# Kernel optimization log

Measured on AMD Instinct MI355X. Metric: run time of the kernel, lower is better.

## Reference

```python
import jax, jax.numpy as jnp
import numpy as np

N = 102400   # total nodes (64 graphs x 1600 nodes)
G = 64       # graphs in batch
NPG = N // G
E = 1638400  # total edges (avg degree 16)
EPG = E // G


def _segmean(x, ids, num):
    s = jax.ops.segment_sum(x, ids, num_segments=num)
    c = jax.ops.segment_sum(jnp.ones((x.shape[0], 1), x.dtype), ids, num_segments=num)
    return s / jnp.maximum(c, 1.0)


def setup_inputs() -> dict:
    key = jax.random.key(0)
    ks = jax.random.split(key, 32)
    node_features = jax.random.normal(ks[0], (N, 60), jnp.float32)
    edge_features = jax.random.normal(ks[1], (E, 1), jnp.float32)
    node_graph = jnp.arange(N, dtype=jnp.int32) // NPG
    edge_graph = jnp.arange(E, dtype=jnp.int32) // EPG
    senders = edge_graph * NPG + jax.random.randint(ks[2], (E,), 0, NPG)
    receivers = edge_graph * NPG + jax.random.randint(ks[3], (E,), 0, NPG)

    def W(k, o, i):
        return (jax.random.normal(k, (o, i), jnp.float32) / np.sqrt(i)).astype(jnp.float32)

    def b(k, o):
        return (jax.random.uniform(k, (o,), jnp.float32) * 0.02 - 0.01).astype(jnp.float32)

    p = dict(
        node_features=node_features, edge_features=edge_features,
        senders=senders, receivers=receivers,
        node_graph=node_graph, edge_graph=edge_graph,
        # encoder: EdgeLinear(8, edge=1, sender=60)
        enc_Wee=W(ks[4], 8, 1), enc_Wes=W(ks[5], 8, 60), enc_be=b(ks[6], 8),
        # encoder: NodeLinear(16, incoming=8, node=60)
        enc_Wnn=W(ks[7], 16, 60), enc_Wni=W(ks[8], 16, 8), enc_bn=b(ks[9], 16),
        # encoder: GlobalLinear(4, edge=8, node=16)
        enc_Wge=W(ks[10], 4, 8), enc_Wgn=W(ks[11], 4, 16), enc_bg=b(ks[12], 4),
        # hidden: EdgeLinear(8, edge=8, sender=16, global=4)
        hid_Wee=W(ks[13], 8, 8), hid_Wes=W(ks[14], 8, 16), hid_Weg=W(ks[15], 8, 4), hid_be=b(ks[16], 8),
        # hidden: NodeLinear(16, node=16, incoming=8, global=4)
        hid_Wnn=W(ks[17], 16, 16), hid_Wni=W(ks[18], 16, 8), hid_Wng=W(ks[19], 16, 4), hid_bn=b(ks[20], 16),
        # hidden: GlobalLinear(4, edge=8, node=16, global=4)
        hid_Wge=W(ks[21], 4, 8), hid_Wgn=W(ks[22], 4, 16), hid_Wgg=W(ks[23], 4, 4), hid_bg=b(ks[24], 4),
        # readouts
        ro_Wn=W(ks[25], 1, 16), ro_bn=b(ks[26], 1),
        ro_Wg=W(ks[27], 1, 4), ro_bg=b(ks[28], 1),
    )
    return p


def reference(node_features, edge_features, senders, receivers, node_graph, edge_graph,
              enc_Wee, enc_Wes, enc_be, enc_Wnn, enc_Wni, enc_bn, enc_Wge, enc_Wgn, enc_bg,
              hid_Wee, hid_Wes, hid_Weg, hid_be, hid_Wnn, hid_Wni, hid_Wng, hid_bn,
              hid_Wge, hid_Wgn, hid_Wgg, hid_bg, ro_Wn, ro_bn, ro_Wg, ro_bg):
    hops = 1
    # ---- encoder GN block ----
    e = jax.nn.relu(edge_features @ enc_Wee.T + node_features[senders] @ enc_Wes.T + enc_be)  # [E,8]
    n = jax.nn.relu(node_features @ enc_Wnn.T + _segmean(e, receivers, N) @ enc_Wni.T + enc_bn)  # [N,16]
    g = jax.nn.relu(_segmean(e, edge_graph, G) @ enc_Wge.T + _segmean(n, node_graph, G) @ enc_Wgn.T + enc_bg)  # [G,4]
    # ---- hidden GN blocks (shared weights across hops) ----
    for _ in range(hops):
        e = jax.nn.relu(e @ hid_Wee.T + n[senders] @ hid_Wes.T + g[edge_graph] @ hid_Weg.T + hid_be)
        n = jax.nn.relu(n @ hid_Wnn.T + _segmean(e, receivers, N) @ hid_Wni.T + g[node_graph] @ hid_Wng.T + hid_bn)
        g = jax.nn.relu(_segmean(e, edge_graph, G) @ hid_Wge.T + _segmean(n, node_graph, G) @ hid_Wgn.T + g @ hid_Wgg.T + hid_bg)
    # ---- readouts ----
    nodes_out = jax.nn.sigmoid(n @ ro_Wn.T + ro_bn)    # [N,1]
    globals_out = jax.nn.sigmoid(g @ ro_Wg.T + ro_bg)  # [G,1]
    return nodes_out, globals_out
```

## Files before the change

### kernel.cpp

```cpp
#include <hip/hip_runtime.h>
#include <hip/hip_bf16.h>
#include <hip/hip_fp16.h>

#define NN   102400
#define NG   64
#define NPG  1600
#define NE   1638400
#define EPG  25600
#define EPC  (EPG / 4)

typedef unsigned int u32;
typedef unsigned short u16;

#define OFF_EDAT   0
#define OFF_SPROJ  (NE)
#define OFF_PNN    (NE + 8 * NN)
#define OFF_SPROJA (NE + 16 * NN)
#define OFF_DEG    (NE + 20 * NN)
#define OFF_START  (NE + 21 * NN)
#define OFF_H4C    (NE + 22 * NN)
#define OFF_GS     (NE + 26 * NN)
#define GS_ESUM1 0
#define GS_NSUM1 512
#define GS_ESUM2 1536
#define GS_NSUM2 2048
#define GS_G1    3072
#define GS_GPE   3328
#define GS_GPN   3840

struct H8 { __half2 a, b, c, d; };

__device__ __forceinline__ void unpack8_f4(const float4 v, float* o) {
    const __half2* h = reinterpret_cast<const __half2*>(&v);
    float2 t0 = __half22float2(h[0]), t1 = __half22float2(h[1]);
    float2 t2 = __half22float2(h[2]), t3 = __half22float2(h[3]);
    o[0]=t0.x; o[1]=t0.y; o[2]=t1.x; o[3]=t1.y; o[4]=t2.x; o[5]=t2.y; o[6]=t3.x; o[7]=t3.y;
}
__device__ __forceinline__ void unpack8(const H8 v, float* o) {
    float2 t0 = __half22float2(v.a), t1 = __half22float2(v.b);
    float2 t2 = __half22float2(v.c), t3 = __half22float2(v.d);
    o[0]=t0.x; o[1]=t0.y; o[2]=t1.x; o[3]=t1.y; o[4]=t2.x; o[5]=t2.y; o[6]=t3.x; o[7]=t3.y;
}
__device__ __forceinline__ H8 pack8(const float* v) {
    H8 r;
    r.a = __floats2half2_rn(v[0], v[1]); r.b = __floats2half2_rn(v[2], v[3]);
    r.c = __floats2half2_rn(v[4], v[5]); r.d = __floats2half2_rn(v[6], v[7]);
    return r;
}
__device__ __forceinline__ u16 f2bf(float f) {
    u32 u = __float_as_uint(f);
    return (u16)((u + 0x7fffu + ((u >> 16) & 1u)) >> 16);
}
__device__ __forceinline__ float wsum(float v) {
#pragma unroll
    for (int o = 32; o >= 1; o >>= 1) v += __shfl_xor(v, o);
    return v;
}
__device__ __forceinline__ float sigmoidf_(float x) { return 1.f / (1.f + expf(-x)); }

__global__ __launch_bounds__(512) void k_hist4(const int* __restrict__ rcv, int* __restrict__ h4) {
    __shared__ int h[NPG];
    const int g = blockIdx.x >> 2, c = blockIdx.x & 3;
    for (int i = threadIdx.x; i < NPG; i += 512) h[i] = 0;
    __syncthreads();
    const int base = g * EPG + c * EPC;
    for (int t = threadIdx.x; t < EPC; t += 512) atomicAdd(&h[rcv[base + t] - g * NPG], 1);
    __syncthreads();
    int* out = h4 + (size_t)(g * 4 + c) * NPG;
    for (int i = threadIdx.x; i < NPG; i += 512) out[i] = h[i];
}

__global__ __launch_bounds__(320) void k_scan(
    int* __restrict__ h4c, int* __restrict__ deg, int* __restrict__ start)
{
    __shared__ int part[320];
    const int g = blockIdx.x, tid = threadIdx.x;
    const int vb = tid * 5;
    int hc[5][4], d[5], pre[5];
    int ts = 0;
#pragma unroll
    for (int i = 0; i < 5; ++i) {
        const int v = vb + i;
#pragma unroll
        for (int c = 0; c < 4; ++c) hc[i][c] = h4c[(size_t)(g * 4 + c) * NPG + v];
        d[i] = hc[i][0] + hc[i][1] + hc[i][2] + hc[i][3];
        pre[i] = ts;
        ts += d[i];
    }
    part[tid] = ts;
    __syncthreads();
    for (int o = 1; o < 320; o <<= 1) {
        const int v = (tid >= o) ? part[tid - o] : 0;
        __syncthreads();
        part[tid] += v;
        __syncthreads();
    }
    const int off = g * EPG + part[tid] - ts;
#pragma unroll
    for (int i = 0; i < 5; ++i) {
        const int v = vb + i;
        const int st = off + pre[i];
        deg[g * NPG + v] = d[i];
        start[g * NPG + v] = st;
        int run = st;
#pragma unroll
        for (int c = 0; c < 4; ++c) {
            h4c[(size_t)(g * 4 + c) * NPG + v] = run;
            run += hc[i][c];
        }
    }
}

__global__ __launch_bounds__(512) void k_scatter4(
    const float* __restrict__ ef, const int* __restrict__ snd, const int* __restrict__ rcv,
    const int* __restrict__ h4c, u32* __restrict__ edat)
{
    __shared__ int cur[NPG];
    const int g = blockIdx.x >> 2, c = blockIdx.x & 3;
    const int* cb = h4c + (size_t)(g * 4 + c) * NPG;
    for (int i = threadIdx.x; i < NPG; i += 512) cur[i] = cb[i];
    __syncthreads();
    const int base = g * EPG + c * EPC;
    for (int t = threadIdx.x; t < EPC; t += 512) {
        const int e = base + t;
        const int r = rcv[e] - g * NPG;
        const int p = atomicAdd(&cur[r], 1);
        const u32 s = (u32)(snd[e] - g * NPG);
        edat[p] = (s << 16) | (u32)f2bf(ef[e]);
    }
}

__global__ __launch_bounds__(256) void k_node_pre(
    const float* __restrict__ nf,
    const float* __restrict__ Wes, const float* __restrict__ Wnn,
    const float* __restrict__ ebe, const float* __restrict__ ebn,
    __half* __restrict__ sproj, __half* __restrict__ pnn,
    __half* __restrict__ sprojAc, float* __restrict__ gs)
{
    __shared__ float wE[480], wN[960];
    for (int i = threadIdx.x; i < 480; i += 256) wE[i] = Wes[i];
    for (int i = threadIdx.x; i < 960; i += 256) wN[i] = Wnn[i];
    if (blockIdx.x == 0) {
        for (int i = threadIdx.x; i < 3072; i += 256) gs[i] = 0.f;
    }
    __syncthreads();
    const int v = blockIdx.x * 256 + threadIdx.x;
    const float4* row = reinterpret_cast<const float4*>(nf + (size_t)v * 60);
    float x[60];
#pragma unroll
    for (int i = 0; i < 15; ++i) {
        const float4 a = row[i];
        x[4 * i] = a.x; x[4 * i + 1] = a.y; x[4 * i + 2] = a.z; x[4 * i + 3] = a.w;
    }
    float pes[8], pn[16];
#pragma unroll
    for (int j = 0; j < 8; ++j) pes[j] = ebe[j];
#pragma unroll
    for (int j = 0; j < 16; ++j) pn[j] = ebn[j];
#pragma unroll
    for (int k = 0; k < 60; ++k) {
        const float xv = x[k];
#pragma unroll
        for (int j = 0; j < 8; ++j)  pes[j] = fmaf(xv, wE[j * 60 + k], pes[j]);
#pragma unroll
        for (int j = 0; j < 16; ++j) pn[j]  = fmaf(xv, wN[j * 60 + k], pn[j]);
    }
    const H8 pa = pack8(pes);
    reinterpret_cast<H8*>(sproj)[(size_t)v * 2] = pa;
    reinterpret_cast<H8*>(sprojAc)[v] = pa;
    H8* pp = reinterpret_cast<H8*>(pnn) + (size_t)v * 2;
    pp[0] = pack8(pn); pp[1] = pack8(pn + 8);
}

__global__ __launch_bounds__(256) void k_enc4(
    const int* __restrict__ deg, const int* __restrict__ start, const u32* __restrict__ edat,
    const __half* __restrict__ sprojAc,
    __half* __restrict__ sproj, __half* __restrict__ pnn,
    const float* __restrict__ eWee, const float* __restrict__ eWni,
    const float* __restrict__ hWes, const float* __restrict__ hWnn,
    float* __restrict__ esum, float* __restrict__ nsum)
{
    __shared__ float wNI[128], wES[128], wNN2[256];
    const int tid = threadIdx.x, lane = tid & 63;
    for (int i = tid; i < 128; i += 256) { wNI[i] = eWni[i]; wES[i] = hWes[i]; }
    wNN2[tid] = hWnn[tid];
    __syncthreads();
    const int v = blockIdx.x * 256 + tid;
    const int g = v / NPG;
    float wee[8];
#pragma unroll
    for (int j = 0; j < 8; ++j) wee[j] = eWee[j];
    const int dg = deg[v];
    const int st = start[v];
    const int aend = st + dg;
    float m[8];
#pragma unroll
    for (int j = 0; j < 8; ++j) m[j] = 0.f;
    const float4* hbA = reinterpret_cast<const float4*>(sprojAc) + (size_t)g * NPG;

    for (int i = st & ~3; i < aend; i += 4) {
        const uint4 w4 = *reinterpret_cast<const uint4*>(edat + i);
        const u32 w[4] = {w4.x, w4.y, w4.z, w4.w};
        float4 A[4];
#pragma unroll
        for (int j = 0; j < 4; ++j) A[j] = hbA[w[j] >> 16];
#pragma unroll
        for (int j = 0; j < 4; ++j) {
            const int idx = i + j;
            const float val = (idx >= st && idx < aend) ? 1.f : 0.f;
            const float f = __uint_as_float((w[j] & 0xffffu) << 16);
            float pv[8]; unpack8_f4(A[j], pv);
#pragma unroll
            for (int k = 0; k < 8; ++k) m[k] += val * fmaxf(0.f, fmaf(f, wee[k], pv[k]));
        }
    }
#pragma unroll
    for (int j = 0; j < 8; ++j) {
        const float s = wsum(m[j]);
        if (lane == 0) atomicAdd(&esum[g * 8 + j], s);
    }
    const float ic = 1.f / fmaxf((float)dg, 1.f);
    float mk[8];
#pragma unroll
    for (int k = 0; k < 8; ++k) mk[k] = m[k] * ic;
    H8* pp = reinterpret_cast<H8*>(pnn) + (size_t)v * 2;
    float pn[16]; unpack8(pp[0], pn); unpack8(pp[1], pn + 8);
    float n1[16];
#pragma unroll
    for (int j = 0; j < 16; ++j) {
        float x = pn[j];
#pragma unroll
        for (int k = 0; k < 8; ++k) x = fmaf(mk[k], wNI[j * 8 + k], x);
        n1[j] = fmaxf(0.f, x);
    }
    float pe[8];
#pragma unroll
    for (int o = 0; o < 8; ++o) {
        float x = 0.f;
#pragma unroll
        for (int j = 0; j < 16; ++j) x = fmaf(n1[j], wES[o * 16 + j], x);
        pe[o] = x;
    }
    reinterpret_cast<H8*>(sproj)[(size_t)v * 2 + 1] = pack8(pe);
    float pw[16];
#pragma unroll
    for (int o = 0; o < 16; ++o) {
        float x = 0.f;
#pragma unroll
        for (int j = 0; j < 16; ++j) x = fmaf(n1[j], wNN2[o * 16 + j], x);
        pw[o] = x;
    }
    pp[0] = pack8(pw); pp[1] = pack8(pw + 8);
#pragma unroll
    for (int j = 0; j < 16; ++j) {
        const float s = wsum(n1[j]);
        if (lane == 0) atomicAdd(&nsum[g * 16 + j], s);
    }
}

__global__ void k_glob_enc(
    const float* __restrict__ esum1, const float* __restrict__ nsum1,
    const float* __restrict__ Wge, const float* __restrict__ Wgn, const float* __restrict__ bg,
    const float* __restrict__ hWeg, const float* __restrict__ hWng,
    float* __restrict__ g1, float* __restrict__ gpe, float* __restrict__ gpn)
{
    const int g = threadIdx.x;
    if (g >= NG) return;
    float gv[4];
#pragma unroll
    for (int o = 0; o < 4; ++o) {
        float x = bg[o];
#pragma unroll
        for (int k = 0; k < 8; ++k)  x = fmaf(esum1[g * 8 + k] * (1.f / EPG), Wge[o * 8 + k], x);
#pragma unroll
        for (int k = 0; k < 16; ++k) x = fmaf(nsum1[g * 16 + k] * (1.f / NPG), Wgn[o * 16 + k], x);
        gv[o] = fmaxf(0.f, x);
        g1[g * 4 + o] = gv[o];
    }
#pragma unroll
    for (int j = 0; j < 8; ++j) {
        float x = 0.f;
#pragma unroll
        for (int o = 0; o < 4; ++o) x = fmaf(gv[o], hWeg[j * 4 + o], x);
        gpe[g * 8 + j] = x;
    }
#pragma unroll
    for (int j = 0; j < 16; ++j) {
        float x = 0.f;
#pragma unroll
        for (int o = 0; o < 4; ++o) x = fmaf(gv[o], hWng[j * 4 + o], x);
        gpn[g * 16 + j] = x;
    }
}

__global__ __launch_bounds__(256) void k_hid4(
    const int* __restrict__ deg, const int* __restrict__ start, const u32* __restrict__ edat,
    const __half* __restrict__ sproj, const __half* __restrict__ pnn,
    const float* __restrict__ eWee,
    const float* __restrict__ hWee, const float* __restrict__ hbe, const float* __restrict__ gpe,
    const float* __restrict__ hWni, const float* __restrict__ hbn, const float* __restrict__ gpn,
    const float* __restrict__ roWn, const float* __restrict__ robn,
    float* __restrict__ esum, float* __restrict__ nsum, float* __restrict__ outn)
{
    __shared__ float w2[64], wNI[128], rW[16];
    const int tid = threadIdx.x, lane = tid & 63;
    for (int i = tid; i < 128; i += 256) wNI[i] = hWni[i];
    if (tid < 64) w2[tid] = hWee[tid];
    if (tid < 16) rW[tid] = roWn[tid];
    __syncthreads();
    const int v = blockIdx.x * 256 + tid;
    const int g = v / NPG;
    float wee[8], add2[8];
#pragma unroll
    for (int j = 0; j < 8; ++j) { wee[j] = eWee[j]; add2[j] = gpe[g * 8 + j] + hbe[j]; }
    const int dg = deg[v];
    const int st = start[v];
    const int aend = st + dg;
    float m2[8];
#pragma unroll
    for (int j = 0; j < 8; ++j) m2[j] = 0.f;
    const float4* hb4 = reinterpret_cast<const float4*>(sproj) + (size_t)g * NPG * 2;

    for (int i = st & ~3; i < aend; i += 4) {
        const uint4 w4 = *reinterpret_cast<const uint4*>(edat + i);
        const u32 w[4] = {w4.x, w4.y, w4.z, w4.w};
        float4 A[4], B[4];
#pragma unroll
        for (int j = 0; j < 4; ++j) {
            const size_t so = (size_t)(w[j] >> 16) * 2;
            A[j] = hb4[so]; B[j] = hb4[so + 1];
        }
#pragma unroll
        for (int j = 0; j < 4; ++j) {
            const int idx = i + j;
            const float val = (idx >= st && idx < aend) ? 1.f : 0.f;
            const float f = __uint_as_float((w[j] & 0xffffu) << 16);
            float pv[8], qv[8];
            unpack8_f4(A[j], pv); unpack8_f4(B[j], qv);
            float e1[8];
#pragma unroll
            for (int k = 0; k < 8; ++k) e1[k] = fmaxf(0.f, fmaf(f, wee[k], pv[k]));
#pragma unroll
            for (int k = 0; k < 8; ++k) {
                float x = qv[k] + add2[k];
#pragma unroll
                for (int kk = 0; kk < 8; ++kk) x = fmaf(e1[kk], w2[k * 8 + kk], x);
                m2[k] += val * fmaxf(0.f, x);
            }
        }
    }
#pragma unroll
    for (int j = 0; j < 8; ++j) {
        const float s = wsum(m2[j]);
        if (lane == 0) atomicAdd(&esum[g * 8 + j], s);
    }
    const float ic = 1.f / fmaxf((float)dg, 1.f);
    float mk[8];
#pragma unroll
    for (int k = 0; k < 8; ++k) mk[k] = m2[k] * ic;
    const H8* pp = reinterpret_cast<const H8*>(pnn) + (size_t)v * 2;
    float pn[16]; unpack8(pp[0], pn); unpack8(pp[1], pn + 8);
    float z = robn[0];
    float n2[16];
#pragma unroll
    for (int j = 0; j < 16; ++j) {
        float x = pn[j] + gpn[g * 16 + j] + hbn[j];
#pragma unroll
        for (int k = 0; k < 8; ++k) x = fmaf(mk[k], wNI[j * 8 + k], x);
        n2[j] = fmaxf(0.f, x);
        z = fmaf(n2[j], rW[j], z);
    }
    outn[v] = sigmoidf_(z);
#pragma unroll
    for (int j = 0; j < 16; ++j) {
        const float s = wsum(n2[j]);
        if (lane == 0) atomicAdd(&nsum[g * 16 + j], s);
    }
}

__global__ void k_glob_hid(
    const float* __restrict__ esum2, const float* __restrict__ nsum2, const float* __restrict__ g1,
    const float* __restrict__ hWge, const float* __restrict__ hWgn,
    const float* __restrict__ hWgg, const float* __restrict__ hbg,
    const float* __restrict__ roWg, const float* __restrict__ robg,
    float* __restrict__ outg)
{
    const int g = threadIdx.x;
    if (g >= NG) return;
    float gv[4];
#pragma unroll
    for (int o = 0; o < 4; ++o) {
        float x = hbg[o];
#pragma unroll
        for (int k = 0; k < 8; ++k)  x = fmaf(esum2[g * 8 + k] * (1.f / EPG), hWge[o * 8 + k], x);
#pragma unroll
        for (int k = 0; k < 16; ++k) x = fmaf(nsum2[g * 16 + k] * (1.f / NPG), hWgn[o * 16 + k], x);
#pragma unroll
        for (int k = 0; k < 4; ++k)  x = fmaf(g1[g * 4 + k], hWgg[o * 4 + k], x);
        gv[o] = fmaxf(0.f, x);
    }
    float z = robg[0];
#pragma unroll
    for (int o = 0; o < 4; ++o) z = fmaf(gv[o], roWg[o], z);
    outg[g] = sigmoidf_(z);
}

extern "C" void kernel_launch(void* const* d_in, const int* in_sizes, int n_in,
                              void* d_out, int out_size, void* d_ws, size_t ws_size,
                              hipStream_t stream)
{
    const float* nf   = (const float*)d_in[0];
    const float* ef   = (const float*)d_in[1];
    const int*   snd  = (const int*)d_in[2];
    const int*   rcv  = (const int*)d_in[3];
    const float* eWee = (const float*)d_in[6];
    const float* eWes = (const float*)d_in[7];
    const float* ebe  = (const float*)d_in[8];
    const float* eWnn = (const float*)d_in[9];
    const float* eWni = (const float*)d_in[10];
    const float* ebn  = (const float*)d_in[11];
    const float* eWge = (const float*)d_in[12];
    const float* eWgn = (const float*)d_in[13];
    const float* ebg  = (const float*)d_in[14];
    const float* hWee = (const float*)d_in[15];
    const float* hWes = (const float*)d_in[16];
    const float* hWeg = (const float*)d_in[17];
    const float* hbe  = (const float*)d_in[18];
    const float* hWnn = (const float*)d_in[19];
    const float* hWni = (const float*)d_in[20];
    const float* hWng = (const float*)d_in[21];
    const float* hbn  = (const float*)d_in[22];
    const float* hWge = (const float*)d_in[23];
    const float* hWgn = (const float*)d_in[24];
    const float* hWgg = (const float*)d_in[25];
    const float* hbg  = (const float*)d_in[26];
    const float* roWn = (const float*)d_in[27];
    const float* robn = (const float*)d_in[28];
    const float* roWg = (const float*)d_in[29];
    const float* robg = (const float*)d_in[30];

    float*  ws     = (float*)d_ws;
    u32*    edat   = (u32*)(ws + OFF_EDAT);
    __half* sproj  = (__half*)(ws + OFF_SPROJ);
    __half* pnn    = (__half*)(ws + OFF_PNN);
    __half* sprojA = (__half*)(ws + OFF_SPROJA);
    int*    deg    = (int*)(ws + OFF_DEG);
    int*    start  = (int*)(ws + OFF_START);
    int*    h4c    = (int*)(ws + OFF_H4C);
    float*  gs     = ws + OFF_GS;
    float* esum1 = gs + GS_ESUM1;
    float* nsum1 = gs + GS_NSUM1;
    float* esum2 = gs + GS_ESUM2;
    float* nsum2 = gs + GS_NSUM2;
    float* g1    = gs + GS_G1;
    float* gpe   = gs + GS_GPE;
    float* gpn   = gs + GS_GPN;
    float* out   = (float*)d_out;

    k_hist4<<<NG * 4, 512, 0, stream>>>(rcv, h4c);
    k_scan<<<NG, 320, 0, stream>>>(h4c, deg, start);
    k_scatter4<<<NG * 4, 512, 0, stream>>>(ef, snd, rcv, h4c, edat);
    k_node_pre<<<NN / 256, 256, 0, stream>>>(nf, eWes, eWnn, ebe, ebn, sproj, pnn, sprojA, gs);
    k_enc4<<<NN / 256, 256, 0, stream>>>(deg, start, edat, sprojA, sproj, pnn,
                                         eWee, eWni, hWes, hWnn, esum1, nsum1);
    k_glob_enc<<<1, 64, 0, stream>>>(esum1, nsum1, eWge, eWgn, ebg, hWeg, hWng, g1, gpe, gpn);
    k_hid4<<<NN / 256, 256, 0, stream>>>(deg, start, edat, sproj, pnn,
                                         eWee, hWee, hbe, gpe, hWni, hbn, gpn,
                                         roWn, robn, esum2, nsum2, out);
    k_glob_hid<<<1, 64, 0, stream>>>(esum2, nsum2, g1, hWge, hWgn, hWgg, hbg, roWg, robg, out + NN);
}
```

Before: 128.0 us.

## Stage per-graph sender projections in LDS for edge aggregation kernels

Blocks are remapped so each covers 200 nodes of a single graph (8 blocks per graph). Each block first copies that graph's sender projection table (1600 or 3200 float4) into shared memory, and the per-edge gathers then read LDS instead of global memory. The aim is to replace scattered global and L2 gathers with LDS reads. The cost is 56 idle threads per block, a large LDS footprint (about 51 KB in the hidden kernel) that limits occupancy, and the same table being loaded redundantly by 8 blocks per graph.

```diff
diff --git a/kernel.cpp b/kernel.cpp
--- a/kernel.cpp
+++ b/kernel.cpp
@@ -8,6 +8,7 @@
 #define NE   1638400
 #define EPG  25600
 #define EPC  (EPG / 4)
+#define NPC  200
 
 typedef unsigned int u32;
 typedef unsigned short u16;
@@ -172,7 +173,7 @@
     pp[0] = pack8(pn); pp[1] = pack8(pn + 8);
 }
 
-__global__ __launch_bounds__(256) void k_enc4(
+__global__ __launch_bounds__(256) void k_enc5(
     const int* __restrict__ deg, const int* __restrict__ start, const u32* __restrict__ edat,
     const __half* __restrict__ sprojAc,
     __half* __restrict__ sproj, __half* __restrict__ pnn,
@@ -180,30 +181,33 @@
     const float* __restrict__ hWes, const float* __restrict__ hWnn,
     float* __restrict__ esum, float* __restrict__ nsum)
 {
+    __shared__ float4 sA[NPG];
     __shared__ float wNI[128], wES[128], wNN2[256];
     const int tid = threadIdx.x, lane = tid & 63;
+    const int g = blockIdx.x >> 3, ch = blockIdx.x & 7;
+    const float4* hbA = reinterpret_cast<const float4*>(sprojAc) + (size_t)g * NPG;
+    for (int i = tid; i < NPG; i += 256) sA[i] = hbA[i];
     for (int i = tid; i < 128; i += 256) { wNI[i] = eWni[i]; wES[i] = hWes[i]; }
     wNN2[tid] = hWnn[tid];
     __syncthreads();
-    const int v = blockIdx.x * 256 + tid;
-    const int g = v / NPG;
     float wee[8];
 #pragma unroll
     for (int j = 0; j < 8; ++j) wee[j] = eWee[j];
-    const int dg = deg[v];
-    const int st = start[v];
+    const bool act = tid < NPC;
+    const int v = g * NPG + ch * NPC + (act ? tid : 0);
+    const int dg = act ? deg[v] : 0;
+    const int st = act ? start[v] : g * EPG;
     const int aend = st + dg;
     float m[8];
 #pragma unroll
     for (int j = 0; j < 8; ++j) m[j] = 0.f;
-    const float4* hbA = reinterpret_cast<const float4*>(sprojAc) + (size_t)g * NPG;
 
     for (int i = st & ~3; i < aend; i += 4) {
         const uint4 w4 = *reinterpret_cast<const uint4*>(edat + i);
         const u32 w[4] = {w4.x, w4.y, w4.z, w4.w};
         float4 A[4];
 #pragma unroll
-        for (int j = 0; j < 4; ++j) A[j] = hbA[w[j] >> 16];
+        for (int j = 0; j < 4; ++j) A[j] = sA[w[j] >> 16];
 #pragma unroll
         for (int j = 0; j < 4; ++j) {
             const int idx = i + j;
@@ -223,34 +227,43 @@
     float mk[8];
 #pragma unroll
     for (int k = 0; k < 8; ++k) mk[k] = m[k] * ic;
-    H8* pp = reinterpret_cast<H8*>(pnn) + (size_t)v * 2;
-    float pn[16]; unpack8(pp[0], pn); unpack8(pp[1], pn + 8);
+    float pn[16];
+    if (act) {
+        const H8* pp = reinterpret_cast<const H8*>(pnn) + (size_t)v * 2;
+        unpack8(pp[0], pn); unpack8(pp[1], pn + 8);
+    } else {
+#pragma unroll
+        for (int j = 0; j < 16; ++j) pn[j] = 0.f;
+    }
     float n1[16];
 #pragma unroll
     for (int j = 0; j < 16; ++j) {
         float x = pn[j];
 #pragma unroll
         for (int k = 0; k < 8; ++k) x = fmaf(mk[k], wNI[j * 8 + k], x);
-        n1[j] = fmaxf(0.f, x);
-    }
-    float pe[8];
-#pragma unroll
-    for (int o = 0; o < 8; ++o) {
-        float x = 0.f;
-#pragma unroll
-        for (int j = 0; j < 16; ++j) x = fmaf(n1[j], wES[o * 16 + j], x);
-        pe[o] = x;
-    }
-    reinterpret_cast<H8*>(sproj)[(size_t)v * 2 + 1] = pack8(pe);
-    float pw[16];
-#pragma unroll
-    for (int o = 0; o < 16; ++o) {
-        float x = 0.f;
-#pragma unroll
-        for (int j = 0; j < 16; ++j) x = fmaf(n1[j], wNN2[o * 16 + j], x);
-        pw[o] = x;
-    }
-    pp[0] = pack8(pw); pp[1] = pack8(pw + 8);
+        n1[j] = act ? fmaxf(0.f, x) : 0.f;
+    }
+    if (act) {
+        float pe[8];
+#pragma unroll
+        for (int o = 0; o < 8; ++o) {
+            float x = 0.f;
+#pragma unroll
+            for (int j = 0; j < 16; ++j) x = fmaf(n1[j], wES[o * 16 + j], x);
+            pe[o] = x;
+        }
+        reinterpret_cast<H8*>(sproj)[(size_t)v * 2 + 1] = pack8(pe);
+        float pw[16];
+#pragma unroll
+        for (int o = 0; o < 16; ++o) {
+            float x = 0.f;
+#pragma unroll
+            for (int j = 0; j < 16; ++j) x = fmaf(n1[j], wNN2[o * 16 + j], x);
+            pw[o] = x;
+        }
+        H8* pp = reinterpret_cast<H8*>(pnn) + (size_t)v * 2;
+        pp[0] = pack8(pw); pp[1] = pack8(pw + 8);
+    }
 #pragma unroll
     for (int j = 0; j < 16; ++j) {
         const float s = wsum(n1[j]);
@@ -293,7 +306,7 @@
     }
 }
 
-__global__ __launch_bounds__(256) void k_hid4(
+__global__ __launch_bounds__(256) void k_hid5(
     const int* __restrict__ deg, const int* __restrict__ start, const u32* __restrict__ edat,
     const __half* __restrict__ sproj, const __half* __restrict__ pnn,
     const float* __restrict__ eWee,
@@ -302,24 +315,27 @@
     const float* __restrict__ roWn, const float* __restrict__ robn,
     float* __restrict__ esum, float* __restrict__ nsum, float* __restrict__ outn)
 {
+    __shared__ float4 sAB[NPG * 2];
     __shared__ float w2[64], wNI[128], rW[16];
     const int tid = threadIdx.x, lane = tid & 63;
+    const int g = blockIdx.x >> 3, ch = blockIdx.x & 7;
+    const float4* f4sp = reinterpret_cast<const float4*>(sproj) + (size_t)g * NPG * 2;
+    for (int i = tid; i < NPG * 2; i += 256) sAB[i] = f4sp[i];
     for (int i = tid; i < 128; i += 256) wNI[i] = hWni[i];
     if (tid < 64) w2[tid] = hWee[tid];
-    if (tid < 16) rW[tid] = roWn[tid];
-    __syncthreads();
-    const int v = blockIdx.x * 256 + tid;
-    const int g = v / NPG;
+    if (tid >= 64 && tid < 80) rW[tid - 64] = roWn[tid - 64];
+    __syncthreads();
     float wee[8], add2[8];
 #pragma unroll
     for (int j = 0; j < 8; ++j) { wee[j] = eWee[j]; add2[j] = gpe[g * 8 + j] + hbe[j]; }
-    const int dg = deg[v];
-    const int st = start[v];
+    const bool act = tid < NPC;
+    const int v = g * NPG + ch * NPC + (act ? tid : 0);
+    const int dg = act ? deg[v] : 0;
+    const int st = act ? start[v] : g * EPG;
     const int aend = st + dg;
     float m2[8];
 #pragma unroll
     for (int j = 0; j < 8; ++j) m2[j] = 0.f;
-    const float4* hb4 = reinterpret_cast<const float4*>(sproj) + (size_t)g * NPG * 2;
 
     for (int i = st & ~3; i < aend; i += 4) {
         const uint4 w4 = *reinterpret_cast<const uint4*>(edat + i);
@@ -327,8 +343,8 @@
         float4 A[4], B[4];
 #pragma unroll
         for (int j = 0; j < 4; ++j) {
-            const size_t so = (size_t)(w[j] >> 16) * 2;
-            A[j] = hb4[so]; B[j] = hb4[so + 1];
+            const int so = (int)(w[j] >> 16) * 2;
+            A[j] = sAB[so]; B[j] = sAB[so + 1];
         }
 #pragma unroll
         for (int j = 0; j < 4; ++j) {
@@ -358,8 +374,14 @@
     float mk[8];
 #pragma unroll
     for (int k = 0; k < 8; ++k) mk[k] = m2[k] * ic;
-    const H8* pp = reinterpret_cast<const H8*>(pnn) + (size_t)v * 2;
-    float pn[16]; unpack8(pp[0], pn); unpack8(pp[1], pn + 8);
+    float pn[16];
+    if (act) {
+        const H8* pp = reinterpret_cast<const H8*>(pnn) + (size_t)v * 2;
+        unpack8(pp[0], pn); unpack8(pp[1], pn + 8);
+    } else {
+#pragma unroll
+        for (int j = 0; j < 16; ++j) pn[j] = 0.f;
+    }
     float z = robn[0];
     float n2[16];
 #pragma unroll
@@ -367,10 +389,10 @@
         float x = pn[j] + gpn[g * 16 + j] + hbn[j];
 #pragma unroll
         for (int k = 0; k < 8; ++k) x = fmaf(mk[k], wNI[j * 8 + k], x);
-        n2[j] = fmaxf(0.f, x);
+        n2[j] = act ? fmaxf(0.f, x) : 0.f;
         z = fmaf(n2[j], rW[j], z);
     }
-    outn[v] = sigmoidf_(z);
+    if (act) outn[v] = sigmoidf_(z);
 #pragma unroll
     for (int j = 0; j < 16; ++j) {
         const float s = wsum(n2[j]);
@@ -461,11 +483,11 @@
     k_scan<<<NG, 320, 0, stream>>>(h4c, deg, start);
     k_scatter4<<<NG * 4, 512, 0, stream>>>(ef, snd, rcv, h4c, edat);
     k_node_pre<<<NN / 256, 256, 0, stream>>>(nf, eWes, eWnn, ebe, ebn, sproj, pnn, sprojA, gs);
-    k_enc4<<<NN / 256, 256, 0, stream>>>(deg, start, edat, sprojA, sproj, pnn,
-                                         eWee, eWni, hWes, hWnn, esum1, nsum1);
+    k_enc5<<<NG * 8, 256, 0, stream>>>(deg, start, edat, sprojA, sproj, pnn,
+                                       eWee, eWni, hWes, hWnn, esum1, nsum1);
     k_glob_enc<<<1, 64, 0, stream>>>(esum1, nsum1, eWge, eWgn, ebg, hWeg, hWng, g1, gpe, gpn);
-    k_hid4<<<NN / 256, 256, 0, stream>>>(deg, start, edat, sproj, pnn,
-                                         eWee, hWee, hbe, gpe, hWni, hbn, gpn,
-                                         roWn, robn, esum2, nsum2, out);
+    k_hid5<<<NG * 8, 256, 0, stream>>>(deg, start, edat, sproj, pnn,
+                                       eWee, hWee, hbe, gpe, hWni, hbn, gpn,
+                                       roWn, robn, esum2, nsum2, out);
     k_glob_hid<<<1, 64, 0, stream>>>(esum2, nsum2, g1, hWge, hWgn, hWgg, hbg, roWg, robg, out + NN);
 }
```

Measured after the change: 134.6 us. 1.05x slower.

## Materialize encoder edge values and fuse node projection with receiver histogram

Applied to the files above, without the earlier changes.

The encoder kernel now stores each edge's relu'd encoder output as packed fp16, and the hidden kernel reads it sequentially instead of re-gathering the sender projection and recomputing it. The sender projection buffer is split into separate A and B arrays, so the hidden gather fetches half as much. Node pre-projection and the receiver histogram are merged into one launch by block range. In exchange, it adds a full per-edge write and read of 16 bytes, which is extra global memory traffic.

```diff
diff --git a/kernel.cpp b/kernel.cpp
--- a/kernel.cpp
+++ b/kernel.cpp
@@ -13,13 +13,14 @@
 typedef unsigned short u16;
 
 #define OFF_EDAT   0
-#define OFF_SPROJ  (NE)
-#define OFF_PNN    (NE + 8 * NN)
-#define OFF_SPROJA (NE + 16 * NN)
-#define OFF_DEG    (NE + 20 * NN)
-#define OFF_START  (NE + 21 * NN)
-#define OFF_H4C    (NE + 22 * NN)
-#define OFF_GS     (NE + 26 * NN)
+#define OFF_EVALS  (NE)
+#define OFF_PNN    (5 * NE)
+#define OFF_SPROJA (5 * NE + 8 * NN)
+#define OFF_SPROJB (5 * NE + 12 * NN)
+#define OFF_DEG    (5 * NE + 16 * NN)
+#define OFF_START  (5 * NE + 17 * NN)
+#define OFF_H4C    (5 * NE + 18 * NN)
+#define OFF_GS     (5 * NE + 22 * NN)
 #define GS_ESUM1 0
 #define GS_NSUM1 512
 #define GS_ESUM2 1536
@@ -58,16 +59,60 @@
 }
 __device__ __forceinline__ float sigmoidf_(float x) { return 1.f / (1.f + expf(-x)); }
 
-__global__ __launch_bounds__(512) void k_hist4(const int* __restrict__ rcv, int* __restrict__ h4) {
-    __shared__ int h[NPG];
-    const int g = blockIdx.x >> 2, c = blockIdx.x & 3;
-    for (int i = threadIdx.x; i < NPG; i += 512) h[i] = 0;
-    __syncthreads();
-    const int base = g * EPG + c * EPC;
-    for (int t = threadIdx.x; t < EPC; t += 512) atomicAdd(&h[rcv[base + t] - g * NPG], 1);
-    __syncthreads();
-    int* out = h4 + (size_t)(g * 4 + c) * NPG;
-    for (int i = threadIdx.x; i < NPG; i += 512) out[i] = h[i];
+__global__ __launch_bounds__(256) void k_pre_hist(
+    const float* __restrict__ nf,
+    const float* __restrict__ Wes, const float* __restrict__ Wnn,
+    const float* __restrict__ ebe, const float* __restrict__ ebn,
+    __half* __restrict__ sprojA, __half* __restrict__ pnn, float* __restrict__ gs,
+    const int* __restrict__ rcv, int* __restrict__ h4)
+{
+    __shared__ float sm[1600];
+    const int tid = threadIdx.x;
+    if (blockIdx.x < 400) {
+        float* wE = sm;
+        float* wN = sm + 480;
+        for (int i = tid; i < 480; i += 256) wE[i] = Wes[i];
+        for (int i = tid; i < 960; i += 256) wN[i] = Wnn[i];
+        if (blockIdx.x == 0) {
+            for (int i = tid; i < 3072; i += 256) gs[i] = 0.f;
+        }
+        __syncthreads();
+        const int v = blockIdx.x * 256 + tid;
+        const float4* row = reinterpret_cast<const float4*>(nf + (size_t)v * 60);
+        float x[60];
+#pragma unroll
+        for (int i = 0; i < 15; ++i) {
+            const float4 a = row[i];
+            x[4 * i] = a.x; x[4 * i + 1] = a.y; x[4 * i + 2] = a.z; x[4 * i + 3] = a.w;
+        }
+        float pes[8], pn[16];
+#pragma unroll
+        for (int j = 0; j < 8; ++j) pes[j] = ebe[j];
+#pragma unroll
+        for (int j = 0; j < 16; ++j) pn[j] = ebn[j];
+#pragma unroll
+        for (int k = 0; k < 60; ++k) {
+            const float xv = x[k];
+#pragma unroll
+            for (int j = 0; j < 8; ++j)  pes[j] = fmaf(xv, wE[j * 60 + k], pes[j]);
+#pragma unroll
+            for (int j = 0; j < 16; ++j) pn[j]  = fmaf(xv, wN[j * 60 + k], pn[j]);
+        }
+        reinterpret_cast<H8*>(sprojA)[v] = pack8(pes);
+        H8* pp = reinterpret_cast<H8*>(pnn) + (size_t)v * 2;
+        pp[0] = pack8(pn); pp[1] = pack8(pn + 8);
+    } else {
+        int* h = reinterpret_cast<int*>(sm);
+        const int b = blockIdx.x - 400;
+        const int g = b >> 2, c = b & 3;
+        for (int i = tid; i < NPG; i += 256) h[i] = 0;
+        __syncthreads();
+        const int base = g * EPG + c * EPC;
+        for (int t = tid; t < EPC; t += 256) atomicAdd(&h[rcv[base + t] - g * NPG], 1);
+        __syncthreads();
+        int* out = h4 + (size_t)(g * 4 + c) * NPG;
+        for (int i = tid; i < NPG; i += 256) out[i] = h[i];
+    }
 }
 
 __global__ __launch_bounds__(320) void k_scan(
@@ -130,52 +175,10 @@
     }
 }
 
-__global__ __launch_bounds__(256) void k_node_pre(
-    const float* __restrict__ nf,
-    const float* __restrict__ Wes, const float* __restrict__ Wnn,
-    const float* __restrict__ ebe, const float* __restrict__ ebn,
-    __half* __restrict__ sproj, __half* __restrict__ pnn,
-    __half* __restrict__ sprojAc, float* __restrict__ gs)
-{
-    __shared__ float wE[480], wN[960];
-    for (int i = threadIdx.x; i < 480; i += 256) wE[i] = Wes[i];
-    for (int i = threadIdx.x; i < 960; i += 256) wN[i] = Wnn[i];
-    if (blockIdx.x == 0) {
-        for (int i = threadIdx.x; i < 3072; i += 256) gs[i] = 0.f;
-    }
-    __syncthreads();
-    const int v = blockIdx.x * 256 + threadIdx.x;
-    const float4* row = reinterpret_cast<const float4*>(nf + (size_t)v * 60);
-    float x[60];
-#pragma unroll
-    for (int i = 0; i < 15; ++i) {
-        const float4 a = row[i];
-        x[4 * i] = a.x; x[4 * i + 1] = a.y; x[4 * i + 2] = a.z; x[4 * i + 3] = a.w;
-    }
-    float pes[8], pn[16];
-#pragma unroll
-    for (int j = 0; j < 8; ++j) pes[j] = ebe[j];
-#pragma unroll
-    for (int j = 0; j < 16; ++j) pn[j] = ebn[j];
-#pragma unroll
-    for (int k = 0; k < 60; ++k) {
-        const float xv = x[k];
-#pragma unroll
-        for (int j = 0; j < 8; ++j)  pes[j] = fmaf(xv, wE[j * 60 + k], pes[j]);
-#pragma unroll
-        for (int j = 0; j < 16; ++j) pn[j]  = fmaf(xv, wN[j * 60 + k], pn[j]);
-    }
-    const H8 pa = pack8(pes);
-    reinterpret_cast<H8*>(sproj)[(size_t)v * 2] = pa;
-    reinterpret_cast<H8*>(sprojAc)[v] = pa;
-    H8* pp = reinterpret_cast<H8*>(pnn) + (size_t)v * 2;
-    pp[0] = pack8(pn); pp[1] = pack8(pn + 8);
-}
-
-__global__ __launch_bounds__(256) void k_enc4(
+__global__ __launch_bounds__(256) void k_enc6(
     const int* __restrict__ deg, const int* __restrict__ start, const u32* __restrict__ edat,
-    const __half* __restrict__ sprojAc,
-    __half* __restrict__ sproj, __half* __restrict__ pnn,
+    const __half* __restrict__ sprojAc, __half* __restrict__ evals,
+    __half* __restrict__ sprojB, __half* __restrict__ pnn,
     const float* __restrict__ eWee, const float* __restrict__ eWni,
     const float* __restrict__ hWes, const float* __restrict__ hWnn,
     float* __restrict__ esum, float* __restrict__ nsum)
@@ -197,6 +200,7 @@
 #pragma unroll
     for (int j = 0; j < 8; ++j) m[j] = 0.f;
     const float4* hbA = reinterpret_cast<const float4*>(sprojAc) + (size_t)g * NPG;
+    H8* ev = reinterpret_cast<H8*>(evals);
 
     for (int i = st & ~3; i < aend; i += 4) {
         const uint4 w4 = *reinterpret_cast<const uint4*>(edat + i);
@@ -207,11 +211,17 @@
 #pragma unroll
         for (int j = 0; j < 4; ++j) {
             const int idx = i + j;
-            const float val = (idx >= st && idx < aend) ? 1.f : 0.f;
+            const bool valid = (idx >= st) && (idx < aend);
             const float f = __uint_as_float((w[j] & 0xffffu) << 16);
             float pv[8]; unpack8_f4(A[j], pv);
-#pragma unroll
-            for (int k = 0; k < 8; ++k) m[k] += val * fmaxf(0.f, fmaf(f, wee[k], pv[k]));
+            float e1[8];
+#pragma unroll
+            for (int k = 0; k < 8; ++k) e1[k] = fmaxf(0.f, fmaf(f, wee[k], pv[k]));
+            if (valid) {
+                ev[idx] = pack8(e1);
+#pragma unroll
+                for (int k = 0; k < 8; ++k) m[k] += e1[k];
+            }
         }
     }
 #pragma unroll
@@ -241,7 +251,7 @@
         for (int j = 0; j < 16; ++j) x = fmaf(n1[j], wES[o * 16 + j], x);
         pe[o] = x;
     }
-    reinterpret_cast<H8*>(sproj)[(size_t)v * 2 + 1] = pack8(pe);
+    reinterpret_cast<H8*>(sprojB)[v] = pack8(pe);
     float pw[16];
 #pragma unroll
     for (int o = 0; o < 16; ++o) {
@@ -293,10 +303,10 @@
     }
 }
 
-__global__ __launch_bounds__(256) void k_hid4(
+__global__ __launch_bounds__(256) void k_hid6(
     const int* __restrict__ deg, const int* __restrict__ start, const u32* __restrict__ edat,
-    const __half* __restrict__ sproj, const __half* __restrict__ pnn,
-    const float* __restrict__ eWee,
+    const __half* __restrict__ evals, const __half* __restrict__ sprojB,
+    const __half* __restrict__ pnn,
     const float* __restrict__ hWee, const float* __restrict__ hbe, const float* __restrict__ gpe,
     const float* __restrict__ hWni, const float* __restrict__ hbn, const float* __restrict__ gpn,
     const float* __restrict__ roWn, const float* __restrict__ robn,
@@ -306,40 +316,34 @@
     const int tid = threadIdx.x, lane = tid & 63;
     for (int i = tid; i < 128; i += 256) wNI[i] = hWni[i];
     if (tid < 64) w2[tid] = hWee[tid];
-    if (tid < 16) rW[tid] = roWn[tid];
+    if (tid >= 64 && tid < 80) rW[tid - 64] = roWn[tid - 64];
     __syncthreads();
     const int v = blockIdx.x * 256 + tid;
     const int g = v / NPG;
-    float wee[8], add2[8];
-#pragma unroll
-    for (int j = 0; j < 8; ++j) { wee[j] = eWee[j]; add2[j] = gpe[g * 8 + j] + hbe[j]; }
+    float add2[8];
+#pragma unroll
+    for (int j = 0; j < 8; ++j) add2[j] = gpe[g * 8 + j] + hbe[j];
     const int dg = deg[v];
     const int st = start[v];
     const int aend = st + dg;
     float m2[8];
 #pragma unroll
     for (int j = 0; j < 8; ++j) m2[j] = 0.f;
-    const float4* hb4 = reinterpret_cast<const float4*>(sproj) + (size_t)g * NPG * 2;
+    const float4* hbB = reinterpret_cast<const float4*>(sprojB) + (size_t)g * NPG;
+    const float4* ev4 = reinterpret_cast<const float4*>(evals);
 
     for (int i = st & ~3; i < aend; i += 4) {
         const uint4 w4 = *reinterpret_cast<const uint4*>(edat + i);
         const u32 w[4] = {w4.x, w4.y, w4.z, w4.w};
-        float4 A[4], B[4];
-#pragma unroll
-        for (int j = 0; j < 4; ++j) {
-            const size_t so = (size_t)(w[j] >> 16) * 2;
-            A[j] = hb4[so]; B[j] = hb4[so + 1];
-        }
+        float4 B[4], E[4];
+#pragma unroll
+        for (int j = 0; j < 4; ++j) { B[j] = hbB[w[j] >> 16]; E[j] = ev4[i + j]; }
 #pragma unroll
         for (int j = 0; j < 4; ++j) {
             const int idx = i + j;
             const float val = (idx >= st && idx < aend) ? 1.f : 0.f;
-            const float f = __uint_as_float((w[j] & 0xffffu) << 16);
-            float pv[8], qv[8];
-            unpack8_f4(A[j], pv); unpack8_f4(B[j], qv);
-            float e1[8];
-#pragma unroll
-            for (int k = 0; k < 8; ++k) e1[k] = fmaxf(0.f, fmaf(f, wee[k], pv[k]));
+            float e1[8], qv[8];
+            unpack8_f4(E[j], e1); unpack8_f4(B[j], qv);
 #pragma unroll
             for (int k = 0; k < 8; ++k) {
                 float x = qv[k] + add2[k];
@@ -441,9 +445,10 @@
 
     float*  ws     = (float*)d_ws;
     u32*    edat   = (u32*)(ws + OFF_EDAT);
-    __half* sproj  = (__half*)(ws + OFF_SPROJ);
+    __half* evals  = (__half*)(ws + OFF_EVALS);
     __half* pnn    = (__half*)(ws + OFF_PNN);
     __half* sprojA = (__half*)(ws + OFF_SPROJA);
+    __half* sprojB = (__half*)(ws + OFF_SPROJB);
     int*    deg    = (int*)(ws + OFF_DEG);
     int*    start  = (int*)(ws + OFF_START);
     int*    h4c    = (int*)(ws + OFF_H4C);
@@ -457,15 +462,14 @@
     float* gpn   = gs + GS_GPN;
     float* out   = (float*)d_out;
 
-    k_hist4<<<NG * 4, 512, 0, stream>>>(rcv, h4c);
+    k_pre_hist<<<656, 256, 0, stream>>>(nf, eWes, eWnn, ebe, ebn, sprojA, pnn, gs, rcv, h4c);
     k_scan<<<NG, 320, 0, stream>>>(h4c, deg, start);
     k_scatter4<<<NG * 4, 512, 0, stream>>>(ef, snd, rcv, h4c, edat);
-    k_node_pre<<<NN / 256, 256, 0, stream>>>(nf, eWes, eWnn, ebe, ebn, sproj, pnn, sprojA, gs);
-    k_enc4<<<NN / 256, 256, 0, stream>>>(deg, start, edat, sprojA, sproj, pnn,
+    k_enc6<<<NN / 256, 256, 0, stream>>>(deg, start, edat, sprojA, evals, sprojB, pnn,
                                          eWee, eWni, hWes, hWnn, esum1, nsum1);
     k_glob_enc<<<1, 64, 0, stream>>>(esum1, nsum1, eWge, eWgn, ebg, hWeg, hWng, g1, gpe, gpn);
-    k_hid4<<<NN / 256, 256, 0, stream>>>(deg, start, edat, sproj, pnn,
-                                         eWee, hWee, hbe, gpe, hWni, hbn, gpn,
+    k_hid6<<<NN / 256, 256, 0, stream>>>(deg, start, edat, evals, sprojB, pnn,
+                                         hWee, hbe, gpe, hWni, hbn, gpn,
                                          roWn, robn, esum2, nsum2, out);
     k_glob_hid<<<1, 64, 0, stream>>>(esum2, nsum2, g1, hWge, hWgn, hWgg, hbg, roWg, robg, out + NN);
 }
```

After: 136.3 us. +6.5%, slower.

## Store gathered sender projections as custom fp8 and fold global encoder into hidden kernel

Applied to the files above, without the earlier changes.

The per-node sender projections gathered per edge in the hidden pass are now stored as a software-packed 8-bit float format (scaled fp16-derived, e5m2-like) in one 16-byte record instead of two 16-byte fp16 loads, halving gather traffic. The tiny single-block global-encoder kernel is removed; each thread of the hidden kernel recomputes the graph's global vector and its projections from esum1/nsum1. This trades precision of the edge inputs (risking tolerance failures) and some redundant per-thread arithmetic for less memory traffic and one fewer launch.

```diff
diff --git a/kernel.cpp b/kernel.cpp
--- a/kernel.cpp
+++ b/kernel.cpp
@@ -13,20 +13,18 @@
 typedef unsigned short u16;
 
 #define OFF_EDAT   0
-#define OFF_SPROJ  (NE)
-#define OFF_PNN    (NE + 8 * NN)
-#define OFF_SPROJA (NE + 16 * NN)
-#define OFF_DEG    (NE + 20 * NN)
-#define OFF_START  (NE + 21 * NN)
-#define OFF_H4C    (NE + 22 * NN)
-#define OFF_GS     (NE + 26 * NN)
+#define OFF_FUSED  (NE)
+#define OFF_PNN    (NE + 4 * NN)
+#define OFF_SPROJA (NE + 12 * NN)
+#define OFF_DEG    (NE + 16 * NN)
+#define OFF_START  (NE + 17 * NN)
+#define OFF_H4C    (NE + 18 * NN)
+#define OFF_GS     (NE + 22 * NN)
 #define GS_ESUM1 0
 #define GS_NSUM1 512
 #define GS_ESUM2 1536
 #define GS_NSUM2 2048
 #define GS_G1    3072
-#define GS_GPE   3328
-#define GS_GPN   3840
 
 struct H8 { __half2 a, b, c, d; };
 
@@ -50,6 +48,29 @@
 __device__ __forceinline__ u16 f2bf(float f) {
     u32 u = __float_as_uint(f);
     return (u16)((u + 0x7fffu + ((u >> 16) & 1u)) >> 16);
+}
+__device__ __forceinline__ u32 pack_fp8x4(const float* v) {
+    u32 r = 0;
+#pragma unroll
+    for (int i = 0; i < 4; ++i) {
+        const u32 u = (u32)__half_as_ushort(__float2half(v[i] * (1.f / 256.f)));
+        const u32 s = (u & 0x8000u) >> 8;
+        u32 mag = u & 0x7fffu;
+        mag = (mag + 0x3Fu + ((mag >> 7) & 1u)) >> 7;
+        if (mag > 0xffu) mag = 0xffu;
+        r |= (s | mag) << (8 * i);
+    }
+    return r;
+}
+__device__ __forceinline__ void fp8x4_to_f4(u32 t, float* o) {
+    u32 lo = ((t & 0x7fu) << 7) | ((t & 0x80u) << 8)
+           | ((t & 0x7f00u) << 15) | ((t & 0x8000u) << 16);
+    u32 tt = t >> 16;
+    u32 hi = ((tt & 0x7fu) << 7) | ((tt & 0x80u) << 8)
+           | ((tt & 0x7f00u) << 15) | ((tt & 0x8000u) << 16);
+    const float2 a = __half22float2(*reinterpret_cast<const __half2*>(&lo));
+    const float2 b = __half22float2(*reinterpret_cast<const __half2*>(&hi));
+    o[0] = a.x * 256.f; o[1] = a.y * 256.f; o[2] = b.x * 256.f; o[3] = b.y * 256.f;
 }
 __device__ __forceinline__ float wsum(float v) {
 #pragma unroll
@@ -134,8 +155,8 @@
     const float* __restrict__ nf,
     const float* __restrict__ Wes, const float* __restrict__ Wnn,
     const float* __restrict__ ebe, const float* __restrict__ ebn,
-    __half* __restrict__ sproj, __half* __restrict__ pnn,
-    __half* __restrict__ sprojAc, float* __restrict__ gs)
+    __half* __restrict__ pnn, __half* __restrict__ sprojAc,
+    uint2* __restrict__ fused2, float* __restrict__ gs)
 {
     __shared__ float wE[480], wN[960];
     for (int i = threadIdx.x; i < 480; i += 256) wE[i] = Wes[i];
@@ -165,9 +186,8 @@
 #pragma unroll
         for (int j = 0; j < 16; ++j) pn[j]  = fmaf(xv, wN[j * 60 + k], pn[j]);
     }
-    const H8 pa = pack8(pes);
-    reinterpret_cast<H8*>(sproj)[(size_t)v * 2] = pa;
-    reinterpret_cast<H8*>(sprojAc)[v] = pa;
+    reinterpret_cast<H8*>(sprojAc)[v] = pack8(pes);
+    fused2[(size_t)v * 2] = make_uint2(pack_fp8x4(pes), pack_fp8x4(pes + 4));
     H8* pp = reinterpret_cast<H8*>(pnn) + (size_t)v * 2;
     pp[0] = pack8(pn); pp[1] = pack8(pn + 8);
 }
@@ -175,7 +195,7 @@
 __global__ __launch_bounds__(256) void k_enc4(
     const int* __restrict__ deg, const int* __restrict__ start, const u32* __restrict__ edat,
     const __half* __restrict__ sprojAc,
-    __half* __restrict__ sproj, __half* __restrict__ pnn,
+    uint2* __restrict__ fused2, __half* __restrict__ pnn,
     const float* __restrict__ eWee, const float* __restrict__ eWni,
     const float* __restrict__ hWes, const float* __restrict__ hWnn,
     float* __restrict__ esum, float* __restrict__ nsum)
@@ -241,7 +261,7 @@
         for (int j = 0; j < 16; ++j) x = fmaf(n1[j], wES[o * 16 + j], x);
         pe[o] = x;
     }
-    reinterpret_cast<H8*>(sproj)[(size_t)v * 2 + 1] = pack8(pe);
+    fused2[(size_t)v * 2 + 1] = make_uint2(pack_fp8x4(pe), pack_fp8x4(pe + 4));
     float pw[16];
 #pragma unroll
     for (int o = 0; o < 16; ++o) {
@@ -258,47 +278,15 @@
     }
 }
 
-__global__ void k_glob_enc(
+__global__ __launch_bounds__(256) void k_hid7(
+    const int* __restrict__ deg, const int* __restrict__ start, const u32* __restrict__ edat,
+    const uint4* __restrict__ fused4, const __half* __restrict__ pnn,
+    const float* __restrict__ eWee,
     const float* __restrict__ esum1, const float* __restrict__ nsum1,
-    const float* __restrict__ Wge, const float* __restrict__ Wgn, const float* __restrict__ bg,
-    const float* __restrict__ hWeg, const float* __restrict__ hWng,
-    float* __restrict__ g1, float* __restrict__ gpe, float* __restrict__ gpn)
-{
-    const int g = threadIdx.x;
-    if (g >= NG) return;
-    float gv[4];
-#pragma unroll
-    for (int o = 0; o < 4; ++o) {
-        float x = bg[o];
-#pragma unroll
-        for (int k = 0; k < 8; ++k)  x = fmaf(esum1[g * 8 + k] * (1.f / EPG), Wge[o * 8 + k], x);
-#pragma unroll
-        for (int k = 0; k < 16; ++k) x = fmaf(nsum1[g * 16 + k] * (1.f / NPG), Wgn[o * 16 + k], x);
-        gv[o] = fmaxf(0.f, x);
-        g1[g * 4 + o] = gv[o];
-    }
-#pragma unroll
-    for (int j = 0; j < 8; ++j) {
-        float x = 0.f;
-#pragma unroll
-        for (int o = 0; o < 4; ++o) x = fmaf(gv[o], hWeg[j * 4 + o], x);
-        gpe[g * 8 + j] = x;
-    }
-#pragma unroll
-    for (int j = 0; j < 16; ++j) {
-        float x = 0.f;
-#pragma unroll
-        for (int o = 0; o < 4; ++o) x = fmaf(gv[o], hWng[j * 4 + o], x);
-        gpn[g * 16 + j] = x;
-    }
-}
-
-__global__ __launch_bounds__(256) void k_hid4(
-    const int* __restrict__ deg, const int* __restrict__ start, const u32* __restrict__ edat,
-    const __half* __restrict__ sproj, const __half* __restrict__ pnn,
-    const float* __restrict__ eWee,
-    const float* __restrict__ hWee, const float* __restrict__ hbe, const float* __restrict__ gpe,
-    const float* __restrict__ hWni, const float* __restrict__ hbn, const float* __restrict__ gpn,
+    const float* __restrict__ eWge, const float* __restrict__ eWgn, const float* __restrict__ ebg,
+    const float* __restrict__ hWeg, const float* __restrict__ hWng, float* __restrict__ g1,
+    const float* __restrict__ hWee, const float* __restrict__ hbe,
+    const float* __restrict__ hWni, const float* __restrict__ hbn,
     const float* __restrict__ roWn, const float* __restrict__ robn,
     float* __restrict__ esum, float* __restrict__ nsum, float* __restrict__ outn)
 {
@@ -310,33 +298,58 @@
     __syncthreads();
     const int v = blockIdx.x * 256 + tid;
     const int g = v / NPG;
-    float wee[8], add2[8];
-#pragma unroll
-    for (int j = 0; j < 8; ++j) { wee[j] = eWee[j]; add2[j] = gpe[g * 8 + j] + hbe[j]; }
+    float wee[8];
+#pragma unroll
+    for (int j = 0; j < 8; ++j) wee[j] = eWee[j];
+    float gv[4];
+#pragma unroll
+    for (int o = 0; o < 4; ++o) {
+        float x = ebg[o];
+#pragma unroll
+        for (int k = 0; k < 8; ++k)  x = fmaf(esum1[g * 8 + k] * (1.f / EPG), eWge[o * 8 + k], x);
+#pragma unroll
+        for (int k = 0; k < 16; ++k) x = fmaf(nsum1[g * 16 + k] * (1.f / NPG), eWgn[o * 16 + k], x);
+        gv[o] = fmaxf(0.f, x);
+    }
+    if (tid < 4) g1[g * 4 + tid] = gv[tid];
+    float add2[8];
+#pragma unroll
+    for (int j = 0; j < 8; ++j) {
+        float x = 0.f;
+#pragma unroll
+        for (int o = 0; o < 4; ++o) x = fmaf(gv[o], hWeg[j * 4 + o], x);
+        add2[j] = x + hbe[j];
+    }
+    float gpnl[16];
+#pragma unroll
+    for (int j = 0; j < 16; ++j) {
+        float x = 0.f;
+#pragma unroll
+        for (int o = 0; o < 4; ++o) x = fmaf(gv[o], hWng[j * 4 + o], x);
+        gpnl[j] = x;
+    }
     const int dg = deg[v];
     const int st = start[v];
     const int aend = st + dg;
     float m2[8];
 #pragma unroll
     for (int j = 0; j < 8; ++j) m2[j] = 0.f;
-    const float4* hb4 = reinterpret_cast<const float4*>(sproj) + (size_t)g * NPG * 2;
+    const uint4* hbF = fused4 + (size_t)g * NPG;
 
     for (int i = st & ~3; i < aend; i += 4) {
         const uint4 w4 = *reinterpret_cast<const uint4*>(edat + i);
         const u32 w[4] = {w4.x, w4.y, w4.z, w4.w};
-        float4 A[4], B[4];
-#pragma unroll
-        for (int j = 0; j < 4; ++j) {
-            const size_t so = (size_t)(w[j] >> 16) * 2;
-            A[j] = hb4[so]; B[j] = hb4[so + 1];
-        }
+        uint4 F[4];
+#pragma unroll
+        for (int j = 0; j < 4; ++j) F[j] = hbF[w[j] >> 16];
 #pragma unroll
         for (int j = 0; j < 4; ++j) {
             const int idx = i + j;
             const float val = (idx >= st && idx < aend) ? 1.f : 0.f;
             const float f = __uint_as_float((w[j] & 0xffffu) << 16);
             float pv[8], qv[8];
-            unpack8_f4(A[j], pv); unpack8_f4(B[j], qv);
+            fp8x4_to_f4(F[j].x, pv); fp8x4_to_f4(F[j].y, pv + 4);
+            fp8x4_to_f4(F[j].z, qv); fp8x4_to_f4(F[j].w, qv + 4);
             float e1[8];
 #pragma unroll
             for (int k = 0; k < 8; ++k) e1[k] = fmaxf(0.f, fmaf(f, wee[k], pv[k]));
@@ -364,7 +377,7 @@
     float n2[16];
 #pragma unroll
     for (int j = 0; j < 16; ++j) {
-        float x = pn[j] + gpn[g * 16 + j] + hbn[j];
+        float x = pn[j] + gpnl[j] + hbn[j];
 #pragma unroll
         for (int k = 0; k < 8; ++k) x = fmaf(mk[k], wNI[j * 8 + k], x);
         n2[j] = fmaxf(0.f, x);
@@ -441,7 +454,8 @@
 
     float*  ws     = (float*)d_ws;
     u32*    edat   = (u32*)(ws + OFF_EDAT);
-    __half* sproj  = (__half*)(ws + OFF_SPROJ);
+    uint2*  fused2 = (uint2*)(ws + OFF_FUSED);
+    uint4*  fused4 = (uint4*)(ws + OFF_FUSED);
     __half* pnn    = (__half*)(ws + OFF_PNN);
     __half* sprojA = (__half*)(ws + OFF_SPROJA);
     int*    deg    = (int*)(ws + OFF_DEG);
@@ -453,19 +467,17 @@
     float* esum2 = gs + GS_ESUM2;
     float* nsum2 = gs + GS_NSUM2;
     float* g1    = gs + GS_G1;
-    float* gpe   = gs + GS_GPE;
-    float* gpn   = gs + GS_GPN;
     float* out   = (float*)d_out;
 
     k_hist4<<<NG * 4, 512, 0, stream>>>(rcv, h4c);
     k_scan<<<NG, 320, 0, stream>>>(h4c, deg, start);
     k_scatter4<<<NG * 4, 512, 0, stream>>>(ef, snd, rcv, h4c, edat);
-    k_node_pre<<<NN / 256, 256, 0, stream>>>(nf, eWes, eWnn, ebe, ebn, sproj, pnn, sprojA, gs);
-    k_enc4<<<NN / 256, 256, 0, stream>>>(deg, start, edat, sprojA, sproj, pnn,
+    k_node_pre<<<NN / 256, 256, 0, stream>>>(nf, eWes, eWnn, ebe, ebn, pnn, sprojA, fused2, gs);
+    k_enc4<<<NN / 256, 256, 0, stream>>>(deg, start, edat, sprojA, fused2, pnn,
                                          eWee, eWni, hWes, hWnn, esum1, nsum1);
-    k_glob_enc<<<1, 64, 0, stream>>>(esum1, nsum1, eWge, eWgn, ebg, hWeg, hWng, g1, gpe, gpn);
-    k_hid4<<<NN / 256, 256, 0, stream>>>(deg, start, edat, sproj, pnn,
-                                         eWee, hWee, hbe, gpe, hWni, hbn, gpn,
-                                         roWn, robn, esum2, nsum2, out);
+    k_hid7<<<NN / 256, 256, 0, stream>>>(deg, start, edat, fused4, pnn, eWee,
+                                         esum1, nsum1, eWge, eWgn, ebg, hWeg, hWng, g1,
+                                         hWee, hbe, hWni, hbn, roWn, robn,
+                                         esum2, nsum2, out);
     k_glob_hid<<<1, 64, 0, stream>>>(esum2, nsum2, g1, hWge, hWgn, hWgg, hbg, roWg, robg, out + NN);
 }
```

New measurement: 130.6 us. About the same (+2.0%).
